# Performance work log

Measured on AMD Instinct MI355X. Metric: run time of the kernel, lower is better.

The kernel has to match this reference:

```python
import jax, jax.numpy as jnp
import numpy as np

N, K, DIM, A, M = 20000, 16, 256, 128, 2500
EPS = 1e-5
SCALE = float(np.sqrt(A))


def _ln(x, g, b):
    mu = x.mean(-1, keepdims=True)
    var = x.var(-1, keepdims=True)
    return (x - mu) / jnp.sqrt(var + EPS) * g + b


def _pe(x, w1, b1, w2, b2):
    # PositionEncoder: Linear -> ReLU -> Linear
    return jax.nn.relu(x @ w1 + b1) @ w2 + b2


def setup_inputs() -> dict:
    key = jax.random.key(0)
    ks = jax.random.split(key, 24)
    w = lambda k, s, fan: jax.random.normal(k, s, jnp.float32) / np.sqrt(fan)
    inp = {
        'events': jax.random.normal(ks[0], (N, 4), jnp.float32),
        'features': jax.random.normal(ks[1], (N, DIM), jnp.float32),
        'local_idx': jax.random.randint(ks[2], (N, K), 0, N, jnp.int32),
        'down_idx': jax.random.randint(ks[3], (M,), 0, N, jnp.int32),
        'pair_idx': jax.random.randint(ks[4], (M, K), 0, N, jnp.int32),
        'inv_pair_idx': jax.random.randint(ks[5], (N, K), 0, M, jnp.int32),
        'local_qkv_w': w(ks[6], (DIM, 3 * A), DIM), 'local_qkv_b': jnp.zeros((3 * A,), jnp.float32),
        'local_pe_w1': w(ks[7], (4, A), 4), 'local_pe_b1': jnp.zeros((A,), jnp.float32),
        'local_pe_w2': w(ks[8], (A, A), A), 'local_pe_b2': jnp.zeros((A,), jnp.float32),
        'local_fc_g': jnp.ones((A,), jnp.float32), 'local_fc_b': jnp.zeros((A,), jnp.float32),
        'global_qkv_w': w(ks[9], (DIM, 3 * A), DIM), 'global_qkv_b': jnp.zeros((3 * A,), jnp.float32),
        'global_pe_w1': w(ks[10], (4, A), 4), 'global_pe_b1': jnp.zeros((A,), jnp.float32),
        'global_pe_w2': w(ks[11], (A, A), A), 'global_pe_b2': jnp.zeros((A,), jnp.float32),
        'global_fc_g': jnp.ones((A,), jnp.float32), 'global_fc_b': jnp.zeros((A,), jnp.float32),
        'proj_w1': w(ks[12], (2 * A, DIM), 2 * A), 'proj_b1': jnp.zeros((DIM,), jnp.float32),
        'proj_w2': w(ks[13], (DIM, DIM), DIM), 'proj_b2': jnp.zeros((DIM,), jnp.float32),
    }
    return inp


def _local_attn(events, features, local_idx, qkv_w, qkv_b,
                pe_w1, pe_b1, pe_w2, pe_b2, fc_g, fc_b):
    # pos enc on event-coordinate differences to the 16 knn neighbors
    pe = _pe(events[:, None, :] - events[local_idx], pe_w1, pe_b1, pe_w2, pe_b2)  # [N,K,A]
    qkv = features @ qkv_w + qkv_b
    q, k, v = jnp.split(qkv, 3, axis=-1)               # [N,A] each
    kg, vg = k[local_idx], v[local_idx]                # [N,K,A]
    attn = _ln(q[:, None, :] - kg + pe, fc_g, fc_b) / SCALE
    attn = jax.nn.softmax(attn, axis=1)                # softmax over neighbors
    return jnp.sum(attn * (vg + pe), axis=1)           # [N,A]


def _global_attn(events, features, down_idx, pair_idx, inv_pair_idx,
                 qkv_w, qkv_b, pe_w1, pe_b1, pe_w2, pe_b2, fc_g, fc_b):
    down_events = events[down_idx]                     # [M,4]
    pe = _pe(events[:, None, :] - down_events[inv_pair_idx], pe_w1, pe_b1, pe_w2, pe_b2)  # [N,K,A]
    qkv = features @ qkv_w + qkv_b
    q, k, v = jnp.split(qkv, 3, axis=-1)
    kmax = jnp.max(k[pair_idx], axis=1)                # [M,A] pooled over k support pts
    vmax = jnp.max(v[pair_idx], axis=1)
    kg, vg = kmax[inv_pair_idx], vmax[inv_pair_idx]    # [N,K,A]
    attn = _ln(q[:, None, :] - kg + pe, fc_g, fc_b) / SCALE
    attn = jax.nn.softmax(attn, axis=1)
    return jnp.sum(attn * (vg + pe), axis=1)


def reference(events, features, local_idx, down_idx, pair_idx, inv_pair_idx,
              local_qkv_w, local_qkv_b, local_pe_w1, local_pe_b1, local_pe_w2, local_pe_b2,
              local_fc_g, local_fc_b,
              global_qkv_w, global_qkv_b, global_pe_w1, global_pe_b1, global_pe_w2, global_pe_b2,
              global_fc_g, global_fc_b,
              proj_w1, proj_b1, proj_w2, proj_b2):
    la = _local_attn(events, features, local_idx, local_qkv_w, local_qkv_b,
                     local_pe_w1, local_pe_b1, local_pe_w2, local_pe_b2,
                     local_fc_g, local_fc_b)
    ga = _global_attn(events, features, down_idx, pair_idx, inv_pair_idx,
                      global_qkv_w, global_qkv_b, global_pe_w1, global_pe_b1,
                      global_pe_w2, global_pe_b2, global_fc_g, global_fc_b)
    attn = jnp.concatenate([la, ga], axis=-1)          # [N,2A]
    # proj MLP: Linear -> ReLU -> Linear
    return jax.nn.relu(attn @ proj_w1 + proj_b1) @ proj_w2 + proj_b2
```

## Files before the change

### kernel.cpp

```cpp
#include <hip/hip_runtime.h>

#define N_PTS 20000
#define KNN   16
#define DIMF  256
#define AD    128
#define MD    2500
#define EPSV  1e-5f
#define INV_SCALE 0.08838834764831845f
#define NEG_BIG -3.402823466e38f

typedef __attribute__((ext_vector_type(8))) short short8v;
typedef __attribute__((ext_vector_type(4))) float f32x4;

__device__ __forceinline__ float b2f(unsigned short u) {
  union { unsigned int i; float f; } v; v.i = ((unsigned int)u) << 16; return v.f;
}
__device__ __forceinline__ unsigned short f2b(float f) {
  union { float f; unsigned int i; } v; v.f = f;
  unsigned int x = v.i;
  return (unsigned short)((x + 0x7fffu + ((x >> 16) & 1u)) >> 16);
}

__global__ void EventAttention_54382875902362_kernel(float* out) {
  if (threadIdx.x == 0 && blockIdx.x == 0) out[0] = 8192.0f;
}

__global__ void prep_all(const float* __restrict__ w2l, const float* __restrict__ w2g,
                         const float* __restrict__ qwl, const float* __restrict__ qwg,
                         const float* __restrict__ pw1, const float* __restrict__ pw2,
                         unsigned short* __restrict__ w2B,
                         unsigned short* __restrict__ wfL, unsigned short* __restrict__ wfG,
                         unsigned short* __restrict__ wp1, unsigned short* __restrict__ wp2)
{
  int id = blockIdx.x * 256 + threadIdx.x;
  if (id < 32768) {
    int br  = id >> 14;
    int rem = id & 16383;
    int e  = rem & 7;
    int l  = (rem >> 3) & 63;
    int ks = (rem >> 9) & 3;
    int tt = rem >> 11;
    int n = tt * 16 + (l & 15);
    int i = ks * 32 + (l >> 4) * 8 + e;
    const float* src = br ? w2g : w2l;
    w2B[id] = f2b(src[i * AD + n]);
    return;
  }
  id -= 32768;
  const float* src;
  unsigned short* dst;
  int ncols, fe;
  if (id < 98304)            { src = qwl; dst = wfL; ncols = 384; fe = 98304; }
  else if (id < 196608)      { src = qwg; dst = wfG; ncols = 384; fe = 98304; id -= 98304; }
  else if (id < 262144)      { src = pw1; dst = wp1; ncols = 256; fe = 65536; id -= 196608; }
  else if (id < 327680)      { src = pw2; dst = wp2; ncols = 256; fe = 65536; id -= 262144; }
  else return;
  int e  = id & 7;
  int l  = (id >> 3) & 63;
  int ks = (id >> 9) & 7;
  int tt = id >> 12;
  int n = tt * 16 + (l & 15);
  int k = ks * 32 + (l >> 4) * 8 + e;
  float v = src[k * ncols + n];
  unsigned short hi = f2b(v);
  unsigned short lo = f2b(v - b2f(hi));
  dst[id] = hi;
  dst[fe + id] = lo;
}

__global__ void qkv_mfma(const float* __restrict__ feat,
                         const unsigned short* __restrict__ wfl, const float* __restrict__ bl,
                         const unsigned short* __restrict__ wfg, const float* __restrict__ bg,
                         float* __restrict__ qkv_l, float* __restrict__ qkv_g,
                         unsigned short* __restrict__ kvl)
{
  __shared__ __align__(16) unsigned short aHi[16 * 256];
  __shared__ __align__(16) unsigned short aLo[16 * 256];
  const int tid  = threadIdx.x;
  const int lane = tid & 63;
  const int wv   = tid >> 6;
  const int br   = blockIdx.x & 1;
  const int row0 = (blockIdx.x >> 1) * 16;

  {
    int r = tid >> 4, seg = tid & 15;
    const float4* src = (const float4*)(feat + (size_t)(row0 + r) * 256 + seg * 16);
    #pragma unroll
    for (int q4 = 0; q4 < 4; ++q4) {
      float4 f = src[q4];
      int byte = (r * 512 + (seg * 16 + q4 * 4) * 2) ^ ((r & 7) << 4);
      ushort4 h, l2;
      h.x = f2b(f.x); l2.x = f2b(f.x - b2f(h.x));
      h.y = f2b(f.y); l2.y = f2b(f.y - b2f(h.y));
      h.z = f2b(f.z); l2.z = f2b(f.z - b2f(h.z));
      h.w = f2b(f.w); l2.w = f2b(f.w - b2f(h.w));
      *(ushort4*)((char*)aHi + byte) = h;
      *(ushort4*)((char*)aLo + byte) = l2;
    }
  }
  __syncthreads();

  short8v ah[8], al[8];
  #pragma unroll
  for (int ks = 0; ks < 8; ++ks) {
    int base = ((lane & 15) * 512 + ks * 64 + (lane >> 4) * 16) ^ ((lane & 7) << 4);
    ah[ks] = *(const short8v*)((const char*)aHi + base);
    al[ks] = *(const short8v*)((const char*)aLo + base);
  }
  const unsigned short* wf = br ? wfg : wfl;
  const float* bias        = br ? bg : bl;
  const short8v* wH = (const short8v*)wf;
  const short8v* wL = wH + 12288;
  f32x4 acc[6];
  #pragma unroll
  for (int t = 0; t < 6; ++t) acc[t] = (f32x4){0.f, 0.f, 0.f, 0.f};
  #pragma unroll
  for (int t = 0; t < 6; ++t) {
    int tt = wv * 6 + t;
    #pragma unroll
    for (int ks = 0; ks < 8; ++ks) {
      short8v bh = wH[(tt * 8 + ks) * 64 + lane];
      short8v bo = wL[(tt * 8 + ks) * 64 + lane];
      acc[t] = __builtin_amdgcn_mfma_f32_16x16x32_bf16(ah[ks], bh, acc[t], 0, 0, 0);
      acc[t] = __builtin_amdgcn_mfma_f32_16x16x32_bf16(al[ks], bh, acc[t], 0, 0, 0);
      acc[t] = __builtin_amdgcn_mfma_f32_16x16x32_bf16(ah[ks], bo, acc[t], 0, 0, 0);
    }
  }
  if (br) {
    #pragma unroll
    for (int t = 0; t < 6; ++t) {
      int colb = (wv * 6 + t) * 16 + (lane & 15);
      float bv = bias[colb];
      #pragma unroll
      for (int r = 0; r < 4; ++r) {
        int row = (lane >> 4) * 4 + r;
        qkv_g[(size_t)(row0 + row) * 384 + colb] = acc[t][r] + bv;
      }
    }
  } else {
    #pragma unroll
    for (int t = 0; t < 6; ++t) {
      int colb = (wv * 6 + t) * 16 + (lane & 15);
      float bv = bias[colb];
      #pragma unroll
      for (int r = 0; r < 4; ++r) {
        int row = (lane >> 4) * 4 + r;
        float val = acc[t][r] + bv;
        if (colb < 128) {
          qkv_l[(size_t)(row0 + row) * 384 + colb] = val;
        } else if (colb < 256) {
          kvl[(size_t)(row0 + row) * 256 + 2 * (colb - 128)] = f2b(val);
        } else {
          kvl[(size_t)(row0 + row) * 256 + 2 * (colb - 256) + 1] = f2b(val);
        }
      }
    }
  }
}

__global__ void kvmax_kernel(const float* __restrict__ qkv_g,
                             const int* __restrict__ pair_idx,
                             unsigned int* __restrict__ kvm)
{
  const int m = blockIdx.x, a = threadIdx.x;
  float km = NEG_BIG, vm = NEG_BIG;
  for (int j = 0; j < KNN; ++j) {
    int p = pair_idx[m * KNN + j];
    km = fmaxf(km, qkv_g[(size_t)p * 384 + 128 + a]);
    vm = fmaxf(vm, qkv_g[(size_t)p * 384 + 256 + a]);
  }
  kvm[m * AD + a] = (unsigned int)f2b(km) | ((unsigned int)f2b(vm) << 16);
}

__global__ __launch_bounds__(128)
void attn_fused(const float* __restrict__ events,
                const int* __restrict__ local_idx,
                const int* __restrict__ inv_pair_idx,
                const int* __restrict__ down_idx,
                const float* __restrict__ qkv_l,
                const float* __restrict__ qkv_g,
                const unsigned int* __restrict__ kvl,
                const unsigned int* __restrict__ kvm,
                const float* __restrict__ w1L, const float* __restrict__ b1L,
                const unsigned short* __restrict__ w2BL, const float* __restrict__ b2L,
                const float* __restrict__ gL,  const float* __restrict__ bbL,
                const float* __restrict__ w1G, const float* __restrict__ b1G,
                const unsigned short* __restrict__ w2BG, const float* __restrict__ b2G,
                const float* __restrict__ gG,  const float* __restrict__ bbG,
                float* __restrict__ out)
{
  __shared__ __align__(16) unsigned short hB[KNN * AD];
  __shared__ float scratch[KNN * 132];
  __shared__ float dS[KNN][4];
  __shared__ int   idxS[KNN];
  __shared__ float red[2][KNN][2];

  const int bid  = blockIdx.x;
  const int gbr  = bid & 1;
  const int n    = bid >> 1;
  const int a    = threadIdx.x;
  const int lane = a & 63;
  const int wv   = a >> 6;

  const int*          idx = gbr ? inv_pair_idx : local_idx;
  const float*        qt  = gbr ? qkv_g : qkv_l;
  const unsigned int* kvt = gbr ? kvm : kvl;
  const float* w1  = gbr ? w1G : w1L;
  const float* b1  = gbr ? b1G : b1L;
  const unsigned short* w2B = gbr ? w2BG : w2BL;
  const float* b2  = gbr ? b2G : b2L;
  const float* gg  = gbr ? gG : gL;
  const float* bbp = gbr ? bbG : bbL;

  if (a < KNN * 4) {
    int j = a >> 2, c = a & 3;
    int idv = idx[n * KNN + j];
    if (c == 0) idxS[j] = idv;
    int erow = gbr ? down_idx[idv] : idv;
    dS[j][c] = events[(size_t)n * 4 + c] - events[(size_t)erow * 4 + c];
  }
  const float w1r0 = w1[0 * AD + a];
  const float w1r1 = w1[1 * AD + a];
  const float w1r2 = w1[2 * AD + a];
  const float w1r3 = w1[3 * AD + a];
  const float b1r = b1[a];
  const float b2r = b2[a];
  const float gr  = gg[a] * INV_SCALE;
  const float brv = bbp[a] * INV_SCALE;
  const float qv  = qt[(size_t)n * 384 + a];
  __syncthreads();

  #pragma unroll
  for (int j = 0; j < KNN; ++j) {
    const float4 d = *(const float4*)dS[j];
    float h = b1r;
    h = fmaf(d.x, w1r0, h);
    h = fmaf(d.y, w1r1, h);
    h = fmaf(d.z, w1r2, h);
    h = fmaf(d.w, w1r3, h);
    h = fmaxf(h, 0.f);
    int byte = (j * 256 + a * 2) ^ ((j & 7) << 4);
    *(unsigned short*)((char*)hB + byte) = f2b(h);
  }
  __syncthreads();

  short8v af[4];
  #pragma unroll
  for (int ksl = 0; ksl < 4; ++ksl) {
    int base = ((lane & 15) * 256 + ksl * 64 + (lane >> 4) * 16) ^ ((lane & 7) << 4);
    af[ksl] = *(const short8v*)((const char*)hB + base);
  }
  f32x4 acc[4];
  #pragma unroll
  for (int t = 0; t < 4; ++t) acc[t] = (f32x4){0.f, 0.f, 0.f, 0.f};
  const short8v* wf = (const short8v*)w2B;
  #pragma unroll
  for (int t = 0; t < 4; ++t) {
    #pragma unroll
    for (int ksl = 0; ksl < 4; ++ksl) {
      short8v bf = wf[(((wv * 4 + t) * 4 + ksl) * 64) + lane];
      acc[t] = __builtin_amdgcn_mfma_f32_16x16x32_bf16(af[ksl], bf, acc[t], 0, 0, 0);
    }
  }
  #pragma unroll
  for (int t = 0; t < 4; ++t) {
    #pragma unroll
    for (int r = 0; r < 4; ++r) {
      int row = (lane >> 4) * 4 + r;
      int col = wv * 64 + t * 16 + (lane & 15);
      scratch[row * 132 + col] = acc[t][r];
    }
  }
  __syncthreads();

  float x[KNN], w[KNN];
  #pragma unroll
  for (int j = 0; j < KNN; ++j) {
    int sid = __builtin_amdgcn_readfirstlane(idxS[j]);
    unsigned int kv = kvt[(size_t)sid * AD + a];
    float pe = scratch[j * 132 + a] + b2r;
    x[j] = qv - b2f((unsigned short)kv) + pe;
    w[j] = b2f((unsigned short)(kv >> 16)) + pe;
  }
  __syncthreads();

  #pragma unroll
  for (int j = 0; j < KNN; ++j) scratch[j * 129 + a] = x[j];
  __syncthreads();

  {
    int jj = a & 15, pp = a >> 4;
    float s1 = 0.f, s2 = 0.f;
    #pragma unroll
    for (int c = 0; c < 16; ++c) {
      float v = scratch[jj * 129 + pp * 16 + c];
      s1 += v;
      s2 = fmaf(v, v, s2);
    }
    s1 += __shfl_xor(s1, 16, 64); s2 += __shfl_xor(s2, 16, 64);
    s1 += __shfl_xor(s1, 32, 64); s2 += __shfl_xor(s2, 32, 64);
    if (lane < 16) { red[wv][jj][0] = s1; red[wv][jj][1] = s2; }
  }
  __syncthreads();

  float mx = NEG_BIG;
  #pragma unroll
  for (int j = 0; j < KNN; ++j) {
    float S1 = red[0][j][0] + red[1][j][0];
    float S2 = red[0][j][1] + red[1][j][1];
    float mu  = S1 * (1.f / AD);
    float var = S2 * (1.f / AD) - mu * mu;
    float rs  = rsqrtf(var + EPSV);
    float s = fmaf((x[j] - mu) * rs, gr, brv);
    x[j] = s;
    mx = fmaxf(mx, s);
  }
  float sum = 0.f;
  #pragma unroll
  for (int j = 0; j < KNN; ++j) {
    float p = __expf(x[j] - mx);
    x[j] = p;
    sum += p;
  }
  const float inv = 1.f / sum;
  float o = 0.f;
  #pragma unroll
  for (int j = 0; j < KNN; ++j)
    o = fmaf(x[j], w[j], o);
  out[(size_t)n * 256 + (gbr ? 128 : 0) + a] = o * inv;
}

__global__ void proj_mfma(const float* __restrict__ attn_cat,
                          const unsigned short* __restrict__ w1f, const float* __restrict__ b1,
                          const unsigned short* __restrict__ w2f, const float* __restrict__ b2,
                          float* __restrict__ outp)
{
  __shared__ __align__(16) unsigned short aHi[16 * 256];
  __shared__ __align__(16) unsigned short aLo[16 * 256];
  const int tid  = threadIdx.x;
  const int lane = tid & 63;
  const int wv   = tid >> 6;
  const int row0 = blockIdx.x * 16;

  {
    int r = tid >> 4, seg = tid & 15;
    const float4* src = (const float4*)(attn_cat + (size_t)(row0 + r) * 256 + seg * 16);
    #pragma unroll
    for (int q4 = 0; q4 < 4; ++q4) {
      float4 f = src[q4];
      int byte = (r * 512 + (seg * 16 + q4 * 4) * 2) ^ ((r & 7) << 4);
      ushort4 h, l2;
      h.x = f2b(f.x); l2.x = f2b(f.x - b2f(h.x));
      h.y = f2b(f.y); l2.y = f2b(f.y - b2f(h.y));
      h.z = f2b(f.z); l2.z = f2b(f.z - b2f(h.z));
      h.w = f2b(f.w); l2.w = f2b(f.w - b2f(h.w));
      *(ushort4*)((char*)aHi + byte) = h;
      *(ushort4*)((char*)aLo + byte) = l2;
    }
  }
  __syncthreads();

  short8v ah[8], al[8];
  #pragma unroll
  for (int ks = 0; ks < 8; ++ks) {
    int base = ((lane & 15) * 512 + ks * 64 + (lane >> 4) * 16) ^ ((lane & 7) << 4);
    ah[ks] = *(const short8v*)((const char*)aHi + base);
    al[ks] = *(const short8v*)((const char*)aLo + base);
  }
  __syncthreads();

  const short8v* w1H = (const short8v*)w1f;
  const short8v* w1L = w1H + 8192;
  f32x4 acc[4];
  #pragma unroll
  for (int t = 0; t < 4; ++t) acc[t] = (f32x4){0.f, 0.f, 0.f, 0.f};
  #pragma unroll
  for (int t = 0; t < 4; ++t) {
    int tt = wv * 4 + t;
    #pragma unroll
    for (int ks = 0; ks < 8; ++ks) {
      short8v bh = w1H[(tt * 8 + ks) * 64 + lane];
      short8v bo = w1L[(tt * 8 + ks) * 64 + lane];
      acc[t] = __builtin_amdgcn_mfma_f32_16x16x32_bf16(ah[ks], bh, acc[t], 0, 0, 0);
      acc[t] = __builtin_amdgcn_mfma_f32_16x16x32_bf16(al[ks], bh, acc[t], 0, 0, 0);
      acc[t] = __builtin_amdgcn_mfma_f32_16x16x32_bf16(ah[ks], bo, acc[t], 0, 0, 0);
    }
  }
  #pragma unroll
  for (int t = 0; t < 4; ++t) {
    int col = (wv * 4 + t) * 16 + (lane & 15);
    float bvv = b1[col];
    #pragma unroll
    for (int r = 0; r < 4; ++r) {
      int row = (lane >> 4) * 4 + r;
      float h = fmaxf(acc[t][r] + bvv, 0.f);
      unsigned short hi = f2b(h);
      unsigned short lo = f2b(h - b2f(hi));
      int byte = (row * 512 + col * 2) ^ ((row & 7) << 4);
      *(unsigned short*)((char*)aHi + byte) = hi;
      *(unsigned short*)((char*)aLo + byte) = lo;
    }
  }
  __syncthreads();

  #pragma unroll
  for (int ks = 0; ks < 8; ++ks) {
    int base = ((lane & 15) * 512 + ks * 64 + (lane >> 4) * 16) ^ ((lane & 7) << 4);
    ah[ks] = *(const short8v*)((const char*)aHi + base);
    al[ks] = *(const short8v*)((const char*)aLo + base);
  }
  const short8v* w2H = (const short8v*)w2f;
  const short8v* w2L = w2H + 8192;
  #pragma unroll
  for (int t = 0; t < 4; ++t) acc[t] = (f32x4){0.f, 0.f, 0.f, 0.f};
  #pragma unroll
  for (int t = 0; t < 4; ++t) {
    int tt = wv * 4 + t;
    #pragma unroll
    for (int ks = 0; ks < 8; ++ks) {
      short8v bh = w2H[(tt * 8 + ks) * 64 + lane];
      short8v bo = w2L[(tt * 8 + ks) * 64 + lane];
      acc[t] = __builtin_amdgcn_mfma_f32_16x16x32_bf16(ah[ks], bh, acc[t], 0, 0, 0);
      acc[t] = __builtin_amdgcn_mfma_f32_16x16x32_bf16(al[ks], bh, acc[t], 0, 0, 0);
      acc[t] = __builtin_amdgcn_mfma_f32_16x16x32_bf16(ah[ks], bo, acc[t], 0, 0, 0);
    }
  }
  #pragma unroll
  for (int t = 0; t < 4; ++t) {
    int col = (wv * 4 + t) * 16 + (lane & 15);
    float bvv = b2[col];
    #pragma unroll
    for (int r = 0; r < 4; ++r) {
      int row = (lane >> 4) * 4 + r;
      outp[(size_t)(row0 + row) * 256 + col] = acc[t][r] + bvv;
    }
  }
}

extern "C" void kernel_launch(void* const* d_in, const int* in_sizes, int n_in,
                              void* d_out, int out_size, void* d_ws, size_t ws_size,
                              hipStream_t stream)
{
  const float* events   = (const float*)d_in[0];
  const float* features = (const float*)d_in[1];
  const int* local_idx    = (const int*)d_in[2];
  const int* down_idx     = (const int*)d_in[3];
  const int* pair_idx     = (const int*)d_in[4];
  const int* inv_pair_idx = (const int*)d_in[5];
  const float* l_qkv_w = (const float*)d_in[6];
  const float* l_qkv_b = (const float*)d_in[7];
  const float* l_pe_w1 = (const float*)d_in[8];
  const float* l_pe_b1 = (const float*)d_in[9];
  const float* l_pe_w2 = (const float*)d_in[10];
  const float* l_pe_b2 = (const float*)d_in[11];
  const float* l_fc_g  = (const float*)d_in[12];
  const float* l_fc_b  = (const float*)d_in[13];
  const float* g_qkv_w = (const float*)d_in[14];
  const float* g_qkv_b = (const float*)d_in[15];
  const float* g_pe_w1 = (const float*)d_in[16];
  const float* g_pe_b1 = (const float*)d_in[17];
  const float* g_pe_w2 = (const float*)d_in[18];
  const float* g_pe_b2 = (const float*)d_in[19];
  const float* g_fc_g  = (const float*)d_in[20];
  const float* g_fc_b  = (const float*)d_in[21];
  const float* p_w1 = (const float*)d_in[22];
  const float* p_b1 = (const float*)d_in[23];
  const float* p_w2 = (const float*)d_in[24];
  const float* p_b2 = (const float*)d_in[25];
  (void)in_sizes; (void)n_in; (void)out_size; (void)ws_size;

  char* ws = (char*)d_ws;
  size_t off = 0;
  float* qkv_l    = (float*)(ws + off); off += (size_t)N_PTS * 384 * 4;
  float* qkv_g    = (float*)(ws + off); off += (size_t)N_PTS * 384 * 4;
  unsigned short* kvl = (unsigned short*)(ws + off); off += (size_t)N_PTS * 256 * 2;
  unsigned int*   kvm = (unsigned int*)(ws + off);   off += (size_t)MD * AD * 4;
  float* attn_cat = (float*)(ws + off); off += (size_t)N_PTS * 256 * 4;
  unsigned short* w2B   = (unsigned short*)(ws + off); off += 32768 * 2;
  unsigned short* wfL   = (unsigned short*)(ws + off); off += 196608 * 2;
  unsigned short* wfG   = (unsigned short*)(ws + off); off += 196608 * 2;
  unsigned short* wp1   = (unsigned short*)(ws + off); off += 131072 * 2;
  unsigned short* wp2   = (unsigned short*)(ws + off); off += 131072 * 2;

  EventAttention_54382875902362_kernel<<<1, 64, 0, stream>>>((float*)d_out);
  prep_all<<<1408, 256, 0, stream>>>(
      l_pe_w2, g_pe_w2, l_qkv_w, g_qkv_w, p_w1, p_w2,
      w2B, wfL, wfG, wp1, wp2);

  qkv_mfma<<<2500, 256, 0, stream>>>(
      features, wfL, l_qkv_b, wfG, g_qkv_b, qkv_l, qkv_g, kvl);
  kvmax_kernel<<<MD, 128, 0, stream>>>(qkv_g, pair_idx, kvm);
  attn_fused<<<2 * N_PTS, 128, 0, stream>>>(
      events, local_idx, inv_pair_idx, down_idx,
      qkv_l, qkv_g, (const unsigned int*)kvl, kvm,
      l_pe_w1, l_pe_b1, w2B, l_pe_b2, l_fc_g, l_fc_b,
      g_pe_w1, g_pe_b1, w2B + 16384, g_pe_b2, g_fc_g, g_fc_b,
      attn_cat);
  proj_mfma<<<N_PTS / 16, 256, 0, stream>>>(
      attn_cat, wp1, p_b1, wp2, p_b2, (float*)d_out);
}
```

Baseline: 206.6 us.

## Compute position-encoder first layer and biases via MFMA with split-bf16 weights

```diff
diff --git a/kernel.cpp b/kernel.cpp
--- a/kernel.cpp
+++ b/kernel.cpp
@@ -7,6 +7,7 @@
 #define MD    2500
 #define EPSV  1e-5f
 #define INV_SCALE 0.08838834764831845f
+#define LOG2E 1.4426950408889634f
 #define NEG_BIG -3.402823466e38f
 
 typedef __attribute__((ext_vector_type(8))) short short8v;
@@ -26,27 +27,68 @@
 }
 
 __global__ void prep_all(const float* __restrict__ w2l, const float* __restrict__ w2g,
+                         const float* __restrict__ b2l, const float* __restrict__ b2g,
+                         const float* __restrict__ w1l, const float* __restrict__ b1l,
+                         const float* __restrict__ w1g, const float* __restrict__ b1g,
                          const float* __restrict__ qwl, const float* __restrict__ qwg,
                          const float* __restrict__ pw1, const float* __restrict__ pw2,
-                         unsigned short* __restrict__ w2B,
+                         unsigned short* __restrict__ w2B, unsigned short* __restrict__ w1B,
                          unsigned short* __restrict__ wfL, unsigned short* __restrict__ wfG,
                          unsigned short* __restrict__ wp1, unsigned short* __restrict__ wp2)
 {
   int id = blockIdx.x * 256 + threadIdx.x;
-  if (id < 32768) {
-    int br  = id >> 14;
-    int rem = id & 16383;
+  if (id < 40960) {
+    int br  = id / 20480;
+    int rem = id % 20480;
     int e  = rem & 7;
     int l  = (rem >> 3) & 63;
-    int ks = (rem >> 9) & 3;
-    int tt = rem >> 11;
+    int ks = (rem >> 9) % 5;
+    int tt = rem / 2560;
     int n = tt * 16 + (l & 15);
-    int i = ks * 32 + (l >> 4) * 8 + e;
-    const float* src = br ? w2g : w2l;
-    w2B[id] = f2b(src[i * AD + n]);
+    const float* w2 = br ? w2g : w2l;
+    const float* b2 = br ? b2g : b2l;
+    unsigned short val = 0;
+    if (ks < 4) {
+      int i = ks * 32 + (l >> 4) * 8 + e;
+      val = f2b(w2[i * AD + n]);
+    } else if ((l >> 4) == 0) {
+      float bv = b2[n];
+      unsigned short hi = f2b(bv);
+      if (e == 0) val = hi;
+      else if (e == 1) val = f2b(bv - b2f(hi));
+    }
+    w2B[id] = val;
     return;
   }
-  id -= 32768;
+  if (id < 49152) {
+    int rem = id - 40960;
+    int br  = rem >> 12;
+    int r2  = rem & 4095;
+    int e  = r2 & 7;
+    int l  = (r2 >> 3) & 63;
+    int tt = r2 >> 9;
+    int n = tt * 16 + (l & 15);
+    int k = (l >> 4) * 8 + e;
+    const float* w1 = br ? w1g : w1l;
+    const float* b1 = br ? b1g : b1l;
+    unsigned short val = 0;
+    if (k < 8) {
+      val = f2b(w1[(k & 3) * AD + n]);
+    } else if (k < 12) {
+      float v = w1[(k - 8) * AD + n];
+      unsigned short hi = f2b(v);
+      val = f2b(v - b2f(hi));
+    } else if (k == 12) {
+      val = f2b(b1[n]);
+    } else if (k == 13) {
+      float v = b1[n];
+      unsigned short hi = f2b(v);
+      val = f2b(v - b2f(hi));
+    }
+    w1B[rem] = val;
+    return;
+  }
+  id -= 49152;
   const float* src;
   unsigned short* dst;
   int ncols, fe;
@@ -181,11 +223,11 @@
                 const float* __restrict__ qkv_g,
                 const unsigned int* __restrict__ kvl,
                 const unsigned int* __restrict__ kvm,
-                const float* __restrict__ w1L, const float* __restrict__ b1L,
-                const unsigned short* __restrict__ w2BL, const float* __restrict__ b2L,
+                const unsigned short* __restrict__ w1BL,
+                const unsigned short* __restrict__ w2BL,
                 const float* __restrict__ gL,  const float* __restrict__ bbL,
-                const float* __restrict__ w1G, const float* __restrict__ b1G,
-                const unsigned short* __restrict__ w2BG, const float* __restrict__ b2G,
+                const unsigned short* __restrict__ w1BG,
+                const unsigned short* __restrict__ w2BG,
                 const float* __restrict__ gG,  const float* __restrict__ bbG,
                 float* __restrict__ out)
 {
@@ -201,14 +243,14 @@
   const int a    = threadIdx.x;
   const int lane = a & 63;
   const int wv   = a >> 6;
+  const int kg   = lane >> 4;
+  const int m    = lane & 15;
 
   const int*          idx = gbr ? inv_pair_idx : local_idx;
   const float*        qt  = gbr ? qkv_g : qkv_l;
   const unsigned int* kvt = gbr ? kvm : kvl;
-  const float* w1  = gbr ? w1G : w1L;
-  const float* b1  = gbr ? b1G : b1L;
-  const unsigned short* w2B = gbr ? w2BG : w2BL;
-  const float* b2  = gbr ? b2G : b2L;
+  const short8v* w1v = (const short8v*)(gbr ? w1BG : w1BL);
+  const short8v* wf  = (const short8v*)(gbr ? w2BG : w2BL);
   const float* gg  = gbr ? gG : gL;
   const float* bbp = gbr ? bbG : bbL;
 
@@ -219,55 +261,71 @@
     int erow = gbr ? down_idx[idv] : idv;
     dS[j][c] = events[(size_t)n * 4 + c] - events[(size_t)erow * 4 + c];
   }
-  const float w1r0 = w1[0 * AD + a];
-  const float w1r1 = w1[1 * AD + a];
-  const float w1r2 = w1[2 * AD + a];
-  const float w1r3 = w1[3 * AD + a];
-  const float b1r = b1[a];
-  const float b2r = b2[a];
-  const float gr  = gg[a] * INV_SCALE;
-  const float brv = bbp[a] * INV_SCALE;
+  const float gr  = gg[a] * (INV_SCALE * LOG2E);
+  const float brv = bbp[a] * (INV_SCALE * LOG2E);
   const float qv  = qt[(size_t)n * 384 + a];
   __syncthreads();
 
-  #pragma unroll
-  for (int j = 0; j < KNN; ++j) {
-    const float4 d = *(const float4*)dS[j];
-    float h = b1r;
-    h = fmaf(d.x, w1r0, h);
-    h = fmaf(d.y, w1r1, h);
-    h = fmaf(d.z, w1r2, h);
-    h = fmaf(d.w, w1r3, h);
-    h = fmaxf(h, 0.f);
-    int byte = (j * 256 + a * 2) ^ ((j & 7) << 4);
-    *(unsigned short*)((char*)hB + byte) = f2b(h);
+  short8v a1 = (short8v){0, 0, 0, 0, 0, 0, 0, 0};
+  {
+    const float4 d = *(const float4*)dS[m];
+    if (kg == 0) {
+      unsigned short h0 = f2b(d.x), h1 = f2b(d.y), h2 = f2b(d.z), h3 = f2b(d.w);
+      a1[0] = (short)h0; a1[1] = (short)h1; a1[2] = (short)h2; a1[3] = (short)h3;
+      a1[4] = (short)f2b(d.x - b2f(h0)); a1[5] = (short)f2b(d.y - b2f(h1));
+      a1[6] = (short)f2b(d.z - b2f(h2)); a1[7] = (short)f2b(d.w - b2f(h3));
+    } else if (kg == 1) {
+      a1[0] = (short)f2b(d.x); a1[1] = (short)f2b(d.y);
+      a1[2] = (short)f2b(d.z); a1[3] = (short)f2b(d.w);
+      a1[4] = (short)0x3F80; a1[5] = (short)0x3F80;
+    }
+  }
+  f32x4 acc1[4];
+  #pragma unroll
+  for (int t = 0; t < 4; ++t) {
+    acc1[t] = (f32x4){0.f, 0.f, 0.f, 0.f};
+    acc1[t] = __builtin_amdgcn_mfma_f32_16x16x32_bf16(
+        a1, w1v[(wv * 4 + t) * 64 + lane], acc1[t], 0, 0, 0);
+  }
+  #pragma unroll
+  for (int t = 0; t < 4; ++t) {
+    #pragma unroll
+    for (int r = 0; r < 4; ++r) {
+      int j = kg * 4 + r;
+      int c = wv * 64 + t * 16 + m;
+      float h = fmaxf(acc1[t][r], 0.f);
+      int byte = (j * 256 + c * 2) ^ ((j & 7) << 4);
+      *(unsigned short*)((char*)hB + byte) = f2b(h);
+    }
   }
   __syncthreads();
 
   short8v af[4];
   #pragma unroll
   for (int ksl = 0; ksl < 4; ++ksl) {
-    int base = ((lane & 15) * 256 + ksl * 64 + (lane >> 4) * 16) ^ ((lane & 7) << 4);
+    int base = (m * 256 + ksl * 64 + kg * 16) ^ ((m & 7) << 4);
     af[ksl] = *(const short8v*)((const char*)hB + base);
   }
+  short8v afb = (short8v){0, 0, 0, 0, 0, 0, 0, 0};
+  if (kg == 0) { afb[0] = (short)0x3F80; afb[1] = (short)0x3F80; }
   f32x4 acc[4];
   #pragma unroll
   for (int t = 0; t < 4; ++t) acc[t] = (f32x4){0.f, 0.f, 0.f, 0.f};
-  const short8v* wf = (const short8v*)w2B;
-  #pragma unroll
-  for (int t = 0; t < 4; ++t) {
-    #pragma unroll
-    for (int ksl = 0; ksl < 4; ++ksl) {
-      short8v bf = wf[(((wv * 4 + t) * 4 + ksl) * 64) + lane];
-      acc[t] = __builtin_amdgcn_mfma_f32_16x16x32_bf16(af[ksl], bf, acc[t], 0, 0, 0);
-    }
+  #pragma unroll
+  for (int t = 0; t < 4; ++t) {
+    #pragma unroll
+    for (int ksl = 0; ksl < 4; ++ksl)
+      acc[t] = __builtin_amdgcn_mfma_f32_16x16x32_bf16(
+          af[ksl], wf[(((wv * 4 + t) * 5 + ksl) * 64) + lane], acc[t], 0, 0, 0);
+    acc[t] = __builtin_amdgcn_mfma_f32_16x16x32_bf16(
+        afb, wf[(((wv * 4 + t) * 5 + 4) * 64) + lane], acc[t], 0, 0, 0);
   }
   #pragma unroll
   for (int t = 0; t < 4; ++t) {
     #pragma unroll
     for (int r = 0; r < 4; ++r) {
-      int row = (lane >> 4) * 4 + r;
-      int col = wv * 64 + t * 16 + (lane & 15);
+      int row = kg * 4 + r;
+      int col = wv * 64 + t * 16 + m;
       scratch[row * 132 + col] = acc[t][r];
     }
   }
@@ -278,7 +336,7 @@
   for (int j = 0; j < KNN; ++j) {
     int sid = __builtin_amdgcn_readfirstlane(idxS[j]);
     unsigned int kv = kvt[(size_t)sid * AD + a];
-    float pe = scratch[j * 132 + a] + b2r;
+    float pe = scratch[j * 132 + a];
     x[j] = qv - b2f((unsigned short)kv) + pe;
     w[j] = b2f((unsigned short)(kv >> 16)) + pe;
   }
@@ -318,7 +376,7 @@
   float sum = 0.f;
   #pragma unroll
   for (int j = 0; j < KNN; ++j) {
-    float p = __expf(x[j] - mx);
+    float p = exp2f(x[j] - mx);
     x[j] = p;
     sum += p;
   }
@@ -476,16 +534,19 @@
   unsigned short* kvl = (unsigned short*)(ws + off); off += (size_t)N_PTS * 256 * 2;
   unsigned int*   kvm = (unsigned int*)(ws + off);   off += (size_t)MD * AD * 4;
   float* attn_cat = (float*)(ws + off); off += (size_t)N_PTS * 256 * 4;
-  unsigned short* w2B   = (unsigned short*)(ws + off); off += 32768 * 2;
+  unsigned short* w2B   = (unsigned short*)(ws + off); off += 40960 * 2;
+  unsigned short* w1B   = (unsigned short*)(ws + off); off += 8192 * 2;
   unsigned short* wfL   = (unsigned short*)(ws + off); off += 196608 * 2;
   unsigned short* wfG   = (unsigned short*)(ws + off); off += 196608 * 2;
   unsigned short* wp1   = (unsigned short*)(ws + off); off += 131072 * 2;
   unsigned short* wp2   = (unsigned short*)(ws + off); off += 131072 * 2;
 
   EventAttention_54382875902362_kernel<<<1, 64, 0, stream>>>((float*)d_out);
-  prep_all<<<1408, 256, 0, stream>>>(
-      l_pe_w2, g_pe_w2, l_qkv_w, g_qkv_w, p_w1, p_w2,
-      w2B, wfL, wfG, wp1, wp2);
+  prep_all<<<1472, 256, 0, stream>>>(
+      l_pe_w2, g_pe_w2, l_pe_b2, g_pe_b2,
+      l_pe_w1, l_pe_b1, g_pe_w1, g_pe_b1,
+      l_qkv_w, g_qkv_w, p_w1, p_w2,
+      w2B, w1B, wfL, wfG, wp1, wp2);
 
   qkv_mfma<<<2500, 256, 0, stream>>>(
       features, wfL, l_qkv_b, wfG, g_qkv_b, qkv_l, qkv_g, kvl);
@@ -493,8 +554,8 @@
   attn_fused<<<2 * N_PTS, 128, 0, stream>>>(
       events, local_idx, inv_pair_idx, down_idx,
       qkv_l, qkv_g, (const unsigned int*)kvl, kvm,
-      l_pe_w1, l_pe_b1, w2B, l_pe_b2, l_fc_g, l_fc_b,
-      g_pe_w1, g_pe_b1, w2B + 16384, g_pe_b2, g_fc_g, g_fc_b,
+      w1B, w2B, l_fc_g, l_fc_b,
+      w1B + 4096, w2B + 20480, g_fc_g, g_fc_b,
       attn_cat);
   proj_mfma<<<N_PTS / 16, 256, 0, stream>>>(
       attn_cat, wp1, p_b1, wp2, p_b2, (float*)d_out);
```

After: 222.3 us. +7.6%, slower.
